# Optimization experiments

Measured on AMD Instinct MI355X. Metric: run time of the kernel, lower is better.

The kernel has to match this reference:

```python
import jax, jax.numpy as jnp
import numpy as np

B, L, E, H = 2, 2048, 1024, 16
D = E // H

def setup_inputs() -> dict:
    key = jax.random.key(0)
    ks = jax.random.split(key, 6)
    values = jax.random.normal(ks[0], (B, L, E), dtype=jnp.float32)
    keys = jax.random.normal(ks[1], (B, L, E), dtype=jnp.float32)
    query = jax.random.normal(ks[2], (B, L, E), dtype=jnp.float32)
    mask = jax.random.randint(ks[3], (B, 1, L, L), 0, 2, dtype=jnp.int32)
    W_out = jax.random.normal(ks[4], (E, E), dtype=jnp.float32) * 0.02
    b_out = jax.random.normal(ks[5], (E,), dtype=jnp.float32) * 0.02
    return {"values": values, "keys": keys, "query": query, "mask": mask,
            "W_out": W_out, "b_out": b_out}

def reference(values, keys, query, mask, W_out, b_out):
    # Note: source module never applies its per-head q/k/v Linear layers;
    # it only reshapes inputs, so we do the same.
    b, l, e = query.shape
    v = values.reshape(b, l, H, D)   # [B, K, H, D]
    k = keys.reshape(b, l, H, D)     # [B, K, H, D]
    q = query.reshape(b, l, H, D)    # [B, Q, H, D]
    # scores[b,h,q,k] = sum_d q[b,q,h,d] * k[b,k,h,d]
    scores = jnp.einsum('bqhd,bkhd->bhqk', q, k)
    scores = jnp.where(mask == 0, jnp.float32(-1e20), scores)
    # source scales by 1/sqrt(embed_size), not head_dim
    attn = jax.nn.softmax(scores / jnp.float32(E ** 0.5), axis=3)
    out = jnp.einsum('bhqk,bkhd->bqhd', attn, v).reshape(b, l, e)
    out = out @ W_out.T + b_out  # torch Linear: x @ W^T + b
    return out
```

## Files before the change

kernel.cpp:

```cpp
#include <hip/hip_runtime.h>
#include <hip/hip_bf16.h>

typedef __bf16 bf16;
typedef __bf16 bf16x8 __attribute__((ext_vector_type(8)));
typedef __bf16 bf16x4 __attribute__((ext_vector_type(4)));
typedef float  f32x4  __attribute__((ext_vector_type(4)));

#define B_ 2
#define L_ 2048
#define E_ 1024
#define H_ 16
#define D_ 64

__global__ __launch_bounds__(256) void cvt_bf16_kernel(const float* __restrict__ in,
                                                       bf16* __restrict__ out, int n4) {
    int i = blockIdx.x * blockDim.x + threadIdx.x;
    int stride = gridDim.x * blockDim.x;
    for (; i < n4; i += stride) {
        float4 f = reinterpret_cast<const float4*>(in)[i];
        bf16x4 o;
        o.x = (bf16)f.x; o.y = (bf16)f.y; o.z = (bf16)f.z; o.w = (bf16)f.w;
        reinterpret_cast<bf16x4*>(out)[i] = o;
    }
}

__global__ __launch_bounds__(256) void vtrans_kernel(const float* __restrict__ v,
                                                     bf16* __restrict__ vt) {
    __shared__ __attribute__((aligned(16))) bf16 tile[64 * 72];
    int bh = blockIdx.y;
    int b = bh >> 4, h = bh & 15;
    int k0 = blockIdx.x * 64;
    int t = threadIdx.x;
    int kk = t >> 2, d0 = (t & 3) * 16;
    const float* src = v + (((size_t)(b * L_ + k0 + kk)) * H_ + h) * D_ + d0;
    float4 f[4];
#pragma unroll
    for (int i = 0; i < 4; i++) f[i] = reinterpret_cast<const float4*>(src)[i];
#pragma unroll
    for (int i = 0; i < 16; i++) {
        float val = reinterpret_cast<const float*>(f)[i];
        tile[(d0 + i) * 72 + kk] = (bf16)val;
    }
    __syncthreads();
    int dd = t >> 2, c = (t & 3) * 16;
    bf16* dst = vt + ((size_t)bh * 64 + dd) * 2048 + k0 + c;
    *reinterpret_cast<uint4*>(dst)     = *reinterpret_cast<const uint4*>(&tile[dd * 72 + c]);
    *reinterpret_cast<uint4*>(dst + 8) = *reinterpret_cast<const uint4*>(&tile[dd * 72 + c + 8]);
}

__global__ __launch_bounds__(256) void mtrans_kernel(const int* __restrict__ mask,
                                                     unsigned char* __restrict__ mt) {
    __shared__ __attribute__((aligned(16))) unsigned char tile[64 * 80];
    int b = blockIdx.z;
    int q0 = blockIdx.x * 64, k0 = blockIdx.y * 64;
    int t = threadIdx.x;
    int qq = t >> 2, kc = (t & 3) * 16;
    const int* src = mask + (size_t)b * L_ * L_ + (size_t)(q0 + qq) * L_ + k0 + kc;
    int4 m[4];
#pragma unroll
    for (int i = 0; i < 4; i++) m[i] = reinterpret_cast<const int4*>(src)[i];
#pragma unroll
    for (int i = 0; i < 16; i++)
        tile[(kc + i) * 80 + qq] = (unsigned char)reinterpret_cast<const int*>(m)[i];
    __syncthreads();
    int kk = t >> 2, qc = (t & 3) * 16;
    unsigned char* dst = mt + (size_t)b * L_ * L_ + (size_t)(k0 + kk) * L_ + q0 + qc;
    *reinterpret_cast<uint4*>(dst) = *reinterpret_cast<const uint4*>(&tile[kk * 80 + qc]);
}

__global__ __launch_bounds__(256) void attn_kernel(const bf16* __restrict__ qb,
                                                   const bf16* __restrict__ kb,
                                                   const bf16* __restrict__ vt,
                                                   const unsigned char* __restrict__ mt,
                                                   bf16* __restrict__ xb) {
    __shared__ __attribute__((aligned(16))) bf16 Qs[128 * 72];
    __shared__ __attribute__((aligned(16))) bf16 Ks[64 * 72];
    __shared__ __attribute__((aligned(16))) bf16 Vs[64 * 72];
    __shared__ __attribute__((aligned(16))) unsigned char Ms[64 * 144];
    __shared__ __attribute__((aligned(16))) bf16 Ps[4][32 * 72];

    const int bh = blockIdx.y, b = bh >> 4, h = bh & 15;
    const int q0 = blockIdx.x * 128;
    const int t = threadIdx.x;
    const int w = t >> 6, lane = t & 63, quad = lane >> 4, ln = lane & 15;

    const float CSCALE = 1.4426950408889634f / 32.0f;

    {
        int r = t >> 1, c0 = (t & 1) * 32;
        const bf16* src = qb + (((size_t)(b * L_ + q0 + r)) * H_ + h) * D_ + c0;
        bf16* dst = &Qs[r * 72 + c0];
#pragma unroll
        for (int i = 0; i < 4; i++)
            *reinterpret_cast<uint4*>(dst + 8 * i) = *reinterpret_cast<const uint4*>(src + 8 * i);
    }

    f32x4 o[2][4], lf[2];
    const f32x4 zero = {0.f, 0.f, 0.f, 0.f};
#pragma unroll
    for (int mi = 0; mi < 2; mi++) {
        lf[mi] = zero;
#pragma unroll
        for (int di = 0; di < 4; di++) o[mi][di] = zero;
    }
    bf16x8 ones;
#pragma unroll
    for (int i = 0; i < 8; i++) ones[i] = (bf16)1.0f;

    for (int kt = 0; kt < L_ / 64; kt++) {
        const int k0 = kt * 64;
        {
            int r = t >> 2, cb = (t & 3) * 16;
            const bf16* ksrc = kb + (((size_t)(b * L_ + k0 + r)) * H_ + h) * D_ + cb;
            *reinterpret_cast<uint4*>(&Ks[r * 72 + cb])     = *reinterpret_cast<const uint4*>(ksrc);
            *reinterpret_cast<uint4*>(&Ks[r * 72 + cb + 8]) = *reinterpret_cast<const uint4*>(ksrc + 8);
            const bf16* vsrc = vt + ((size_t)bh * 64 + r) * 2048 + k0 + cb;
            *reinterpret_cast<uint4*>(&Vs[r * 72 + cb])     = *reinterpret_cast<const uint4*>(vsrc);
            *reinterpret_cast<uint4*>(&Vs[r * 72 + cb + 8]) = *reinterpret_cast<const uint4*>(vsrc + 8);
            const unsigned char* msrc = mt + (size_t)b * L_ * L_ + (size_t)(k0 + r) * L_ + q0 + (t & 3) * 32;
            *reinterpret_cast<uint4*>(&Ms[r * 144 + (t & 3) * 32])      = *reinterpret_cast<const uint4*>(msrc);
            *reinterpret_cast<uint4*>(&Ms[r * 144 + (t & 3) * 32 + 16]) = *reinterpret_cast<const uint4*>(msrc + 16);
        }
        __syncthreads();

        f32x4 s[2][4];
#pragma unroll
        for (int mi = 0; mi < 2; mi++)
#pragma unroll
            for (int ni = 0; ni < 4; ni++) s[mi][ni] = zero;

        bf16x8 aq[2][2];
#pragma unroll
        for (int mi = 0; mi < 2; mi++)
#pragma unroll
            for (int dc = 0; dc < 2; dc++)
                aq[mi][dc] = *reinterpret_cast<const bf16x8*>(&Qs[(w * 32 + mi * 16 + ln) * 72 + (dc * 4 + quad) * 8]);
#pragma unroll
        for (int ni = 0; ni < 4; ni++) {
            bf16x8 bk0 = *reinterpret_cast<const bf16x8*>(&Ks[(ni * 16 + ln) * 72 + quad * 8]);
            bf16x8 bk1 = *reinterpret_cast<const bf16x8*>(&Ks[(ni * 16 + ln) * 72 + (4 + quad) * 8]);
#pragma unroll
            for (int mi = 0; mi < 2; mi++) {
                s[mi][ni] = __builtin_amdgcn_mfma_f32_16x16x32_bf16(aq[mi][0], bk0, s[mi][ni], 0, 0, 0);
                s[mi][ni] = __builtin_amdgcn_mfma_f32_16x16x32_bf16(aq[mi][1], bk1, s[mi][ni], 0, 0, 0);
            }
        }

#pragma unroll
        for (int mi = 0; mi < 2; mi++)
#pragma unroll
            for (int ni = 0; ni < 4; ni++) {
                unsigned int mw = *reinterpret_cast<const unsigned int*>(
                    &Ms[(ni * 16 + ln) * 144 + (w * 8 + mi * 4 + quad) * 4]);
#pragma unroll
                for (int r = 0; r < 4; r++) {
                    float p = __builtin_amdgcn_exp2f(s[mi][ni][r] * CSCALE) *
                              (float)((mw >> (8 * r)) & 255u);
                    Ps[w][(mi * 16 + quad * 4 + r) * 72 + ni * 16 + ln] = (bf16)p;
                }
            }

        bf16x8 ap[2][2];
#pragma unroll
        for (int mi = 0; mi < 2; mi++)
#pragma unroll
            for (int kc = 0; kc < 2; kc++)
                ap[mi][kc] = *reinterpret_cast<const bf16x8*>(&Ps[w][(mi * 16 + ln) * 72 + (kc * 4 + quad) * 8]);
#pragma unroll
        for (int di = 0; di < 4; di++) {
            bf16x8 bv0 = *reinterpret_cast<const bf16x8*>(&Vs[(di * 16 + ln) * 72 + quad * 8]);
            bf16x8 bv1 = *reinterpret_cast<const bf16x8*>(&Vs[(di * 16 + ln) * 72 + (4 + quad) * 8]);
#pragma unroll
            for (int mi = 0; mi < 2; mi++) {
                o[mi][di] = __builtin_amdgcn_mfma_f32_16x16x32_bf16(ap[mi][0], bv0, o[mi][di], 0, 0, 0);
                o[mi][di] = __builtin_amdgcn_mfma_f32_16x16x32_bf16(ap[mi][1], bv1, o[mi][di], 0, 0, 0);
            }
        }
#pragma unroll
        for (int mi = 0; mi < 2; mi++) {
            lf[mi] = __builtin_amdgcn_mfma_f32_16x16x32_bf16(ap[mi][0], ones, lf[mi], 0, 0, 0);
            lf[mi] = __builtin_amdgcn_mfma_f32_16x16x32_bf16(ap[mi][1], ones, lf[mi], 0, 0, 0);
        }
        __syncthreads();
    }

#pragma unroll
    for (int mi = 0; mi < 2; mi++)
#pragma unroll
        for (int di = 0; di < 4; di++)
#pragma unroll
            for (int r = 0; r < 4; r++) {
                int row = w * 32 + mi * 16 + quad * 4 + r;
                int col = di * 16 + ln;
                float val = o[mi][di][r] / lf[mi][r];
                xb[((size_t)(b * L_ + q0 + row)) * E_ + h * 64 + col] = (bf16)val;
            }
}

__global__ __launch_bounds__(256) void proj_kernel(const bf16* __restrict__ xb,
                                                   const bf16* __restrict__ wb,
                                                   const float* __restrict__ bias,
                                                   float* __restrict__ out) {
    __shared__ __attribute__((aligned(16))) bf16 As[128 * 72];
    __shared__ __attribute__((aligned(16))) bf16 Bs[128 * 72];
    const int n0 = blockIdx.x * 128, m0 = blockIdx.y * 128;
    const int t = threadIdx.x;
    const int w = t >> 6, lane = t & 63, quad = lane >> 4, ln = lane & 15;
    const int wm = w >> 1, wn = w & 1;

    f32x4 c[4][4];
    const f32x4 zero = {0.f, 0.f, 0.f, 0.f};
#pragma unroll
    for (int mi = 0; mi < 4; mi++)
#pragma unroll
        for (int ni = 0; ni < 4; ni++) c[mi][ni] = zero;

    for (int kt = 0; kt < E_ / 64; kt++) {
        const int k0 = kt * 64;
        {
            int r = t >> 1, c0 = (t & 1) * 32;
            const bf16* asrc = xb + (size_t)(m0 + r) * E_ + k0 + c0;
            const bf16* bsrc = wb + (size_t)(n0 + r) * E_ + k0 + c0;
#pragma unroll
            for (int i = 0; i < 4; i++)
                *reinterpret_cast<uint4*>(&As[r * 72 + c0 + 8 * i]) = *reinterpret_cast<const uint4*>(asrc + 8 * i);
#pragma unroll
            for (int i = 0; i < 4; i++)
                *reinterpret_cast<uint4*>(&Bs[r * 72 + c0 + 8 * i]) = *reinterpret_cast<const uint4*>(bsrc + 8 * i);
        }
        __syncthreads();
#pragma unroll
        for (int kc = 0; kc < 2; kc++) {
            bf16x8 a[4], bb[4];
#pragma unroll
            for (int mi = 0; mi < 4; mi++)
                a[mi] = *reinterpret_cast<const bf16x8*>(&As[(wm * 64 + mi * 16 + ln) * 72 + (kc * 4 + quad) * 8]);
#pragma unroll
            for (int ni = 0; ni < 4; ni++)
                bb[ni] = *reinterpret_cast<const bf16x8*>(&Bs[(wn * 64 + ni * 16 + ln) * 72 + (kc * 4 + quad) * 8]);
#pragma unroll
            for (int mi = 0; mi < 4; mi++)
#pragma unroll
                for (int ni = 0; ni < 4; ni++)
                    c[mi][ni] = __builtin_amdgcn_mfma_f32_16x16x32_bf16(a[mi], bb[ni], c[mi][ni], 0, 0, 0);
        }
        __syncthreads();
    }
#pragma unroll
    for (int ni = 0; ni < 4; ni++) {
        float bv = bias[n0 + wn * 64 + ni * 16 + ln];
#pragma unroll
        for (int mi = 0; mi < 4; mi++)
#pragma unroll
            for (int r = 0; r < 4; r++) {
                int row = m0 + wm * 64 + mi * 16 + quad * 4 + r;
                int col = n0 + wn * 64 + ni * 16 + ln;
                out[(size_t)row * E_ + col] = c[mi][ni][r] + bv;
            }
    }
}

extern "C" void kernel_launch(void* const* d_in, const int* in_sizes, int n_in,
                              void* d_out, int out_size, void* d_ws, size_t ws_size,
                              hipStream_t stream) {
    (void)in_sizes; (void)n_in; (void)out_size; (void)ws_size;
    const float* values = (const float*)d_in[0];
    const float* keys   = (const float*)d_in[1];
    const float* query  = (const float*)d_in[2];
    const int*   mask   = (const int*)d_in[3];
    const float* W_out  = (const float*)d_in[4];
    const float* b_out  = (const float*)d_in[5];
    float* out = (float*)d_out;

    char* ws = (char*)d_ws;
    bf16* qb = (bf16*)(ws);
    bf16* kb = (bf16*)(ws + 8388608);
    bf16* vt = (bf16*)(ws + 16777216);
    bf16* wb = (bf16*)(ws + 25165824);
    unsigned char* mt = (unsigned char*)(ws + 27262976);
    bf16* xb = (bf16*)(ws + 35651584);

    cvt_bf16_kernel<<<1024, 256, 0, stream>>>(query, qb, (B_ * L_ * E_) / 4);
    cvt_bf16_kernel<<<1024, 256, 0, stream>>>(keys,  kb, (B_ * L_ * E_) / 4);
    cvt_bf16_kernel<<<1024, 256, 0, stream>>>(W_out, wb, (E_ * E_) / 4);
    vtrans_kernel<<<dim3(L_ / 64, B_ * H_), 256, 0, stream>>>(values, vt);
    mtrans_kernel<<<dim3(L_ / 64, L_ / 64, B_), 256, 0, stream>>>(mask, mt);
    attn_kernel<<<dim3(L_ / 128, B_ * H_), 256, 0, stream>>>(qb, kb, vt, mt, xb);
    proj_kernel<<<dim3(E_ / 128, (B_ * L_) / 128), 256, 0, stream>>>(xb, wb, b_out, out);
}
```

Baseline: 235.5 us.

## Bit-pack mask, swizzle LDS tiles, fold softmax scale into Q, shrink tiles

The mask is packed into a bitmask with one bit per query, which cuts attention-kernel mask traffic by about 8x compared with the byte layout. LDS tiles switch from padded rows to an XOR swizzle. The softmax scale is now applied to Q during the bf16 conversion instead of per score. Attention and projection tiles shrink to 64 rows with a launch bound requesting 4 blocks, giving more blocks and higher occupancy at the cost of less data reuse per block.

```diff
diff --git a/kernel.cpp b/kernel.cpp
--- a/kernel.cpp
+++ b/kernel.cpp
@@ -12,14 +12,19 @@
 #define H_ 16
 #define D_ 64
 
+__device__ __forceinline__ int swz(int r, int c) {
+    return r * 64 + (((c ^ (r & 7)) & 7) << 3);
+}
+
 __global__ __launch_bounds__(256) void cvt_bf16_kernel(const float* __restrict__ in,
-                                                       bf16* __restrict__ out, int n4) {
+                                                       bf16* __restrict__ out, int n4, float scale) {
     int i = blockIdx.x * blockDim.x + threadIdx.x;
     int stride = gridDim.x * blockDim.x;
     for (; i < n4; i += stride) {
         float4 f = reinterpret_cast<const float4*>(in)[i];
         bf16x4 o;
-        o.x = (bf16)f.x; o.y = (bf16)f.y; o.z = (bf16)f.z; o.w = (bf16)f.w;
+        o.x = (bf16)(f.x * scale); o.y = (bf16)(f.y * scale);
+        o.z = (bf16)(f.z * scale); o.w = (bf16)(f.w * scale);
         reinterpret_cast<bf16x4*>(out)[i] = o;
     }
 }
@@ -49,7 +54,7 @@
 }
 
 __global__ __launch_bounds__(256) void mtrans_kernel(const int* __restrict__ mask,
-                                                     unsigned char* __restrict__ mt) {
+                                                     unsigned short* __restrict__ mt) {
     __shared__ __attribute__((aligned(16))) unsigned char tile[64 * 80];
     int b = blockIdx.z;
     int q0 = blockIdx.x * 64, k0 = blockIdx.y * 64;
@@ -63,198 +68,180 @@
     for (int i = 0; i < 16; i++)
         tile[(kc + i) * 80 + qq] = (unsigned char)reinterpret_cast<const int*>(m)[i];
     __syncthreads();
-    int kk = t >> 2, qc = (t & 3) * 16;
-    unsigned char* dst = mt + (size_t)b * L_ * L_ + (size_t)(k0 + kk) * L_ + q0 + qc;
-    *reinterpret_cast<uint4*>(dst) = *reinterpret_cast<const uint4*>(&tile[kk * 80 + qc]);
-}
-
-__global__ __launch_bounds__(256) void attn_kernel(const bf16* __restrict__ qb,
-                                                   const bf16* __restrict__ kb,
-                                                   const bf16* __restrict__ vt,
-                                                   const unsigned char* __restrict__ mt,
-                                                   bf16* __restrict__ xb) {
-    __shared__ __attribute__((aligned(16))) bf16 Qs[128 * 72];
-    __shared__ __attribute__((aligned(16))) bf16 Ks[64 * 72];
-    __shared__ __attribute__((aligned(16))) bf16 Vs[64 * 72];
-    __shared__ __attribute__((aligned(16))) unsigned char Ms[64 * 144];
-    __shared__ __attribute__((aligned(16))) bf16 Ps[4][32 * 72];
+    int kk = t >> 2, q16 = (t & 3) * 16;
+    unsigned int v = 0;
+#pragma unroll
+    for (int i = 0; i < 16; i++)
+        v |= ((unsigned int)(tile[kk * 80 + q16 + i] & 1)) << i;
+    mt[((size_t)(b * L_) + k0 + kk) * (L_ / 16) + (q0 >> 4) + (t & 3)] = (unsigned short)v;
+}
+
+__global__ __launch_bounds__(256, 4) void attn_kernel(const bf16* __restrict__ qb,
+                                                      const bf16* __restrict__ kb,
+                                                      const bf16* __restrict__ vt,
+                                                      const unsigned int* __restrict__ mt,
+                                                      bf16* __restrict__ xb) {
+    __shared__ __attribute__((aligned(16))) bf16 Qs[64 * 64];
+    __shared__ __attribute__((aligned(16))) bf16 Ks[64 * 64];
+    __shared__ __attribute__((aligned(16))) bf16 Vs[64 * 64];
+    __shared__ __attribute__((aligned(16))) bf16 Ps[4][16 * 72];
+    __shared__ unsigned int Ms32[64 * 2];
 
     const int bh = blockIdx.y, b = bh >> 4, h = bh & 15;
-    const int q0 = blockIdx.x * 128;
+    const int q0 = blockIdx.x * 64;
     const int t = threadIdx.x;
     const int w = t >> 6, lane = t & 63, quad = lane >> 4, ln = lane & 15;
-
-    const float CSCALE = 1.4426950408889634f / 32.0f;
+    const int r_ = t >> 2, c2 = (t & 3) * 2;
 
     {
-        int r = t >> 1, c0 = (t & 1) * 32;
-        const bf16* src = qb + (((size_t)(b * L_ + q0 + r)) * H_ + h) * D_ + c0;
-        bf16* dst = &Qs[r * 72 + c0];
-#pragma unroll
-        for (int i = 0; i < 4; i++)
-            *reinterpret_cast<uint4*>(dst + 8 * i) = *reinterpret_cast<const uint4*>(src + 8 * i);
-    }
-
-    f32x4 o[2][4], lf[2];
+        const bf16* src = qb + (((size_t)(b * L_ + q0 + r_)) * H_ + h) * D_ + c2 * 8;
+        *reinterpret_cast<uint4*>(&Qs[swz(r_, c2)])     = *reinterpret_cast<const uint4*>(src);
+        *reinterpret_cast<uint4*>(&Qs[swz(r_, c2 + 1)]) = *reinterpret_cast<const uint4*>(src + 8);
+    }
+    __syncthreads();
+
+    bf16x8 aq[2];
+#pragma unroll
+    for (int dc = 0; dc < 2; dc++)
+        aq[dc] = *reinterpret_cast<const bf16x8*>(&Qs[swz(w * 16 + ln, dc * 4 + quad)]);
+
+    f32x4 o[4], lf;
     const f32x4 zero = {0.f, 0.f, 0.f, 0.f};
-#pragma unroll
-    for (int mi = 0; mi < 2; mi++) {
-        lf[mi] = zero;
-#pragma unroll
-        for (int di = 0; di < 4; di++) o[mi][di] = zero;
-    }
+    lf = zero;
+#pragma unroll
+    for (int di = 0; di < 4; di++) o[di] = zero;
     bf16x8 ones;
 #pragma unroll
     for (int i = 0; i < 8; i++) ones[i] = (bf16)1.0f;
+
+    const int mshift = (w & 1) * 16 + quad * 4;
+    const int mword = (w >> 1);
 
     for (int kt = 0; kt < L_ / 64; kt++) {
         const int k0 = kt * 64;
         {
-            int r = t >> 2, cb = (t & 3) * 16;
-            const bf16* ksrc = kb + (((size_t)(b * L_ + k0 + r)) * H_ + h) * D_ + cb;
-            *reinterpret_cast<uint4*>(&Ks[r * 72 + cb])     = *reinterpret_cast<const uint4*>(ksrc);
-            *reinterpret_cast<uint4*>(&Ks[r * 72 + cb + 8]) = *reinterpret_cast<const uint4*>(ksrc + 8);
-            const bf16* vsrc = vt + ((size_t)bh * 64 + r) * 2048 + k0 + cb;
-            *reinterpret_cast<uint4*>(&Vs[r * 72 + cb])     = *reinterpret_cast<const uint4*>(vsrc);
-            *reinterpret_cast<uint4*>(&Vs[r * 72 + cb + 8]) = *reinterpret_cast<const uint4*>(vsrc + 8);
-            const unsigned char* msrc = mt + (size_t)b * L_ * L_ + (size_t)(k0 + r) * L_ + q0 + (t & 3) * 32;
-            *reinterpret_cast<uint4*>(&Ms[r * 144 + (t & 3) * 32])      = *reinterpret_cast<const uint4*>(msrc);
-            *reinterpret_cast<uint4*>(&Ms[r * 144 + (t & 3) * 32 + 16]) = *reinterpret_cast<const uint4*>(msrc + 16);
-        }
-        __syncthreads();
-
-        f32x4 s[2][4];
-#pragma unroll
-        for (int mi = 0; mi < 2; mi++)
-#pragma unroll
-            for (int ni = 0; ni < 4; ni++) s[mi][ni] = zero;
-
-        bf16x8 aq[2][2];
-#pragma unroll
-        for (int mi = 0; mi < 2; mi++)
-#pragma unroll
-            for (int dc = 0; dc < 2; dc++)
-                aq[mi][dc] = *reinterpret_cast<const bf16x8*>(&Qs[(w * 32 + mi * 16 + ln) * 72 + (dc * 4 + quad) * 8]);
+            const bf16* ksrc = kb + (((size_t)(b * L_ + k0 + r_)) * H_ + h) * D_ + c2 * 8;
+            *reinterpret_cast<uint4*>(&Ks[swz(r_, c2)])     = *reinterpret_cast<const uint4*>(ksrc);
+            *reinterpret_cast<uint4*>(&Ks[swz(r_, c2 + 1)]) = *reinterpret_cast<const uint4*>(ksrc + 8);
+            const bf16* vsrc = vt + ((size_t)bh * 64 + r_) * 2048 + k0 + c2 * 8;
+            *reinterpret_cast<uint4*>(&Vs[swz(r_, c2)])     = *reinterpret_cast<const uint4*>(vsrc);
+            *reinterpret_cast<uint4*>(&Vs[swz(r_, c2 + 1)]) = *reinterpret_cast<const uint4*>(vsrc + 8);
+            if (t < 128) {
+                int k = t >> 1, half = t & 1;
+                Ms32[k * 2 + half] = mt[((size_t)(b * L_) + k0 + k) * (L_ / 32) + (q0 >> 5) + half];
+            }
+        }
+        __syncthreads();
+
+        f32x4 s[4];
+#pragma unroll
+        for (int ni = 0; ni < 4; ni++) s[ni] = zero;
 #pragma unroll
         for (int ni = 0; ni < 4; ni++) {
-            bf16x8 bk0 = *reinterpret_cast<const bf16x8*>(&Ks[(ni * 16 + ln) * 72 + quad * 8]);
-            bf16x8 bk1 = *reinterpret_cast<const bf16x8*>(&Ks[(ni * 16 + ln) * 72 + (4 + quad) * 8]);
-#pragma unroll
-            for (int mi = 0; mi < 2; mi++) {
-                s[mi][ni] = __builtin_amdgcn_mfma_f32_16x16x32_bf16(aq[mi][0], bk0, s[mi][ni], 0, 0, 0);
-                s[mi][ni] = __builtin_amdgcn_mfma_f32_16x16x32_bf16(aq[mi][1], bk1, s[mi][ni], 0, 0, 0);
-            }
-        }
-
-#pragma unroll
-        for (int mi = 0; mi < 2; mi++)
-#pragma unroll
-            for (int ni = 0; ni < 4; ni++) {
-                unsigned int mw = *reinterpret_cast<const unsigned int*>(
-                    &Ms[(ni * 16 + ln) * 144 + (w * 8 + mi * 4 + quad) * 4]);
-#pragma unroll
-                for (int r = 0; r < 4; r++) {
-                    float p = __builtin_amdgcn_exp2f(s[mi][ni][r] * CSCALE) *
-                              (float)((mw >> (8 * r)) & 255u);
-                    Ps[w][(mi * 16 + quad * 4 + r) * 72 + ni * 16 + ln] = (bf16)p;
-                }
-            }
-
-        bf16x8 ap[2][2];
-#pragma unroll
-        for (int mi = 0; mi < 2; mi++)
-#pragma unroll
-            for (int kc = 0; kc < 2; kc++)
-                ap[mi][kc] = *reinterpret_cast<const bf16x8*>(&Ps[w][(mi * 16 + ln) * 72 + (kc * 4 + quad) * 8]);
+#pragma unroll
+            for (int dc = 0; dc < 2; dc++) {
+                bf16x8 bk = *reinterpret_cast<const bf16x8*>(&Ks[swz(ni * 16 + ln, dc * 4 + quad)]);
+                s[ni] = __builtin_amdgcn_mfma_f32_16x16x32_bf16(aq[dc], bk, s[ni], 0, 0, 0);
+            }
+        }
+
+#pragma unroll
+        for (int ni = 0; ni < 4; ni++) {
+            unsigned int mw = Ms32[(ni * 16 + ln) * 2 + mword];
+#pragma unroll
+            for (int r = 0; r < 4; r++) {
+                float p = __builtin_amdgcn_exp2f(s[ni][r]) *
+                          (float)((mw >> (mshift + r)) & 1u);
+                Ps[w][(quad * 4 + r) * 72 + ni * 16 + ln] = (bf16)p;
+            }
+        }
+
+        bf16x8 ap[2];
+#pragma unroll
+        for (int kc = 0; kc < 2; kc++)
+            ap[kc] = *reinterpret_cast<const bf16x8*>(&Ps[w][ln * 72 + (kc * 4 + quad) * 8]);
 #pragma unroll
         for (int di = 0; di < 4; di++) {
-            bf16x8 bv0 = *reinterpret_cast<const bf16x8*>(&Vs[(di * 16 + ln) * 72 + quad * 8]);
-            bf16x8 bv1 = *reinterpret_cast<const bf16x8*>(&Vs[(di * 16 + ln) * 72 + (4 + quad) * 8]);
-#pragma unroll
-            for (int mi = 0; mi < 2; mi++) {
-                o[mi][di] = __builtin_amdgcn_mfma_f32_16x16x32_bf16(ap[mi][0], bv0, o[mi][di], 0, 0, 0);
-                o[mi][di] = __builtin_amdgcn_mfma_f32_16x16x32_bf16(ap[mi][1], bv1, o[mi][di], 0, 0, 0);
-            }
-        }
-#pragma unroll
-        for (int mi = 0; mi < 2; mi++) {
-            lf[mi] = __builtin_amdgcn_mfma_f32_16x16x32_bf16(ap[mi][0], ones, lf[mi], 0, 0, 0);
-            lf[mi] = __builtin_amdgcn_mfma_f32_16x16x32_bf16(ap[mi][1], ones, lf[mi], 0, 0, 0);
-        }
-        __syncthreads();
-    }
-
-#pragma unroll
-    for (int mi = 0; mi < 2; mi++)
-#pragma unroll
-        for (int di = 0; di < 4; di++)
-#pragma unroll
-            for (int r = 0; r < 4; r++) {
-                int row = w * 32 + mi * 16 + quad * 4 + r;
-                int col = di * 16 + ln;
-                float val = o[mi][di][r] / lf[mi][r];
-                xb[((size_t)(b * L_ + q0 + row)) * E_ + h * 64 + col] = (bf16)val;
-            }
-}
-
-__global__ __launch_bounds__(256) void proj_kernel(const bf16* __restrict__ xb,
-                                                   const bf16* __restrict__ wb,
-                                                   const float* __restrict__ bias,
-                                                   float* __restrict__ out) {
-    __shared__ __attribute__((aligned(16))) bf16 As[128 * 72];
-    __shared__ __attribute__((aligned(16))) bf16 Bs[128 * 72];
-    const int n0 = blockIdx.x * 128, m0 = blockIdx.y * 128;
+#pragma unroll
+            for (int kc = 0; kc < 2; kc++) {
+                bf16x8 bv = *reinterpret_cast<const bf16x8*>(&Vs[swz(di * 16 + ln, kc * 4 + quad)]);
+                o[di] = __builtin_amdgcn_mfma_f32_16x16x32_bf16(ap[kc], bv, o[di], 0, 0, 0);
+            }
+        }
+#pragma unroll
+        for (int kc = 0; kc < 2; kc++)
+            lf = __builtin_amdgcn_mfma_f32_16x16x32_bf16(ap[kc], ones, lf, 0, 0, 0);
+        __syncthreads();
+    }
+
+#pragma unroll
+    for (int r = 0; r < 4; r++) {
+        float rinv = 1.0f / lf[r];
+        int q = w * 16 + quad * 4 + r;
+#pragma unroll
+        for (int di = 0; di < 4; di++) {
+            xb[((size_t)(b * L_ + q0 + q)) * E_ + h * 64 + di * 16 + ln] =
+                (bf16)(o[di][r] * rinv);
+        }
+    }
+}
+
+__global__ __launch_bounds__(256, 4) void proj_kernel(const bf16* __restrict__ xb,
+                                                      const bf16* __restrict__ wb,
+                                                      const float* __restrict__ bias,
+                                                      float* __restrict__ out) {
+    __shared__ __attribute__((aligned(16))) bf16 As[64 * 64];
+    __shared__ __attribute__((aligned(16))) bf16 Bs[64 * 64];
+    const int n0 = blockIdx.x * 64, m0 = blockIdx.y * 64;
     const int t = threadIdx.x;
     const int w = t >> 6, lane = t & 63, quad = lane >> 4, ln = lane & 15;
     const int wm = w >> 1, wn = w & 1;
-
-    f32x4 c[4][4];
+    const int r_ = t >> 2, c2 = (t & 3) * 2;
+
+    f32x4 c[2][2];
     const f32x4 zero = {0.f, 0.f, 0.f, 0.f};
 #pragma unroll
-    for (int mi = 0; mi < 4; mi++)
-#pragma unroll
-        for (int ni = 0; ni < 4; ni++) c[mi][ni] = zero;
+    for (int mi = 0; mi < 2; mi++)
+#pragma unroll
+        for (int ni = 0; ni < 2; ni++) c[mi][ni] = zero;
 
     for (int kt = 0; kt < E_ / 64; kt++) {
         const int k0 = kt * 64;
         {
-            int r = t >> 1, c0 = (t & 1) * 32;
-            const bf16* asrc = xb + (size_t)(m0 + r) * E_ + k0 + c0;
-            const bf16* bsrc = wb + (size_t)(n0 + r) * E_ + k0 + c0;
-#pragma unroll
-            for (int i = 0; i < 4; i++)
-                *reinterpret_cast<uint4*>(&As[r * 72 + c0 + 8 * i]) = *reinterpret_cast<const uint4*>(asrc + 8 * i);
-#pragma unroll
-            for (int i = 0; i < 4; i++)
-                *reinterpret_cast<uint4*>(&Bs[r * 72 + c0 + 8 * i]) = *reinterpret_cast<const uint4*>(bsrc + 8 * i);
+            const bf16* asrc = xb + (size_t)(m0 + r_) * E_ + k0 + c2 * 8;
+            const bf16* bsrc = wb + (size_t)(n0 + r_) * E_ + k0 + c2 * 8;
+            *reinterpret_cast<uint4*>(&As[swz(r_, c2)])     = *reinterpret_cast<const uint4*>(asrc);
+            *reinterpret_cast<uint4*>(&As[swz(r_, c2 + 1)]) = *reinterpret_cast<const uint4*>(asrc + 8);
+            *reinterpret_cast<uint4*>(&Bs[swz(r_, c2)])     = *reinterpret_cast<const uint4*>(bsrc);
+            *reinterpret_cast<uint4*>(&Bs[swz(r_, c2 + 1)]) = *reinterpret_cast<const uint4*>(bsrc + 8);
         }
         __syncthreads();
 #pragma unroll
         for (int kc = 0; kc < 2; kc++) {
-            bf16x8 a[4], bb[4];
-#pragma unroll
-            for (int mi = 0; mi < 4; mi++)
-                a[mi] = *reinterpret_cast<const bf16x8*>(&As[(wm * 64 + mi * 16 + ln) * 72 + (kc * 4 + quad) * 8]);
-#pragma unroll
-            for (int ni = 0; ni < 4; ni++)
-                bb[ni] = *reinterpret_cast<const bf16x8*>(&Bs[(wn * 64 + ni * 16 + ln) * 72 + (kc * 4 + quad) * 8]);
-#pragma unroll
-            for (int mi = 0; mi < 4; mi++)
-#pragma unroll
-                for (int ni = 0; ni < 4; ni++)
+            bf16x8 a[2], bb[2];
+#pragma unroll
+            for (int mi = 0; mi < 2; mi++)
+                a[mi] = *reinterpret_cast<const bf16x8*>(&As[swz(wm * 32 + mi * 16 + ln, kc * 4 + quad)]);
+#pragma unroll
+            for (int ni = 0; ni < 2; ni++)
+                bb[ni] = *reinterpret_cast<const bf16x8*>(&Bs[swz(wn * 32 + ni * 16 + ln, kc * 4 + quad)]);
+#pragma unroll
+            for (int mi = 0; mi < 2; mi++)
+#pragma unroll
+                for (int ni = 0; ni < 2; ni++)
                     c[mi][ni] = __builtin_amdgcn_mfma_f32_16x16x32_bf16(a[mi], bb[ni], c[mi][ni], 0, 0, 0);
         }
         __syncthreads();
     }
 #pragma unroll
-    for (int ni = 0; ni < 4; ni++) {
-        float bv = bias[n0 + wn * 64 + ni * 16 + ln];
-#pragma unroll
-        for (int mi = 0; mi < 4; mi++)
+    for (int ni = 0; ni < 2; ni++) {
+        float bv = bias[n0 + wn * 32 + ni * 16 + ln];
+#pragma unroll
+        for (int mi = 0; mi < 2; mi++)
 #pragma unroll
             for (int r = 0; r < 4; r++) {
-                int row = m0 + wm * 64 + mi * 16 + quad * 4 + r;
-                int col = n0 + wn * 64 + ni * 16 + ln;
+                int row = m0 + wm * 32 + mi * 16 + quad * 4 + r;
+                int col = n0 + wn * 32 + ni * 16 + ln;
                 out[(size_t)row * E_ + col] = c[mi][ni][r] + bv;
             }
     }
@@ -277,14 +264,16 @@
     bf16* kb = (bf16*)(ws + 8388608);
     bf16* vt = (bf16*)(ws + 16777216);
     bf16* wb = (bf16*)(ws + 25165824);
-    unsigned char* mt = (unsigned char*)(ws + 27262976);
+    unsigned short* mt = (unsigned short*)(ws + 27262976);
     bf16* xb = (bf16*)(ws + 35651584);
 
-    cvt_bf16_kernel<<<1024, 256, 0, stream>>>(query, qb, (B_ * L_ * E_) / 4);
-    cvt_bf16_kernel<<<1024, 256, 0, stream>>>(keys,  kb, (B_ * L_ * E_) / 4);
-    cvt_bf16_kernel<<<1024, 256, 0, stream>>>(W_out, wb, (E_ * E_) / 4);
+    const float CSCALE = 1.4426950408889634f / 32.0f;
+
+    cvt_bf16_kernel<<<1024, 256, 0, stream>>>(query, qb, (B_ * L_ * E_) / 4, CSCALE);
+    cvt_bf16_kernel<<<1024, 256, 0, stream>>>(keys,  kb, (B_ * L_ * E_) / 4, 1.0f);
+    cvt_bf16_kernel<<<64, 256, 0, stream>>>(W_out, wb, (E_ * E_) / 4, 1.0f);
     vtrans_kernel<<<dim3(L_ / 64, B_ * H_), 256, 0, stream>>>(values, vt);
     mtrans_kernel<<<dim3(L_ / 64, L_ / 64, B_), 256, 0, stream>>>(mask, mt);
-    attn_kernel<<<dim3(L_ / 128, B_ * H_), 256, 0, stream>>>(qb, kb, vt, mt, xb);
-    proj_kernel<<<dim3(E_ / 128, (B_ * L_) / 128), 256, 0, stream>>>(xb, wb, b_out, out);
-}
+    attn_kernel<<<dim3(L_ / 64, B_ * H_), 256, 0, stream>>>(qb, kb, vt, (const unsigned int*)mt, xb);
+    proj_kernel<<<dim3(E_ / 64, (B_ * L_) / 64), 256, 0, stream>>>(xb, wb, b_out, out);
+}
```

New measurement: 228.8 us. 1.03x faster.
